# Optimization experiments

Hardware: AMD Instinct MI355X
Metric: run time of the kernel (lower is better)

The kernel has to match this reference:

```python
import jax, jax.numpy as jnp
import numpy as np

UNITS = 1024
IN_DIM = 1024
BATCH = 4096


def setup_inputs() -> dict:
    key = jax.random.key(0)
    ks = jax.random.split(key, 11)
    C = UNITS + IN_DIM  # concat dim
    glorot = lambda k, shp: jax.random.uniform(k, shp, jnp.float32, -1.0, 1.0) * np.sqrt(6.0 / (shp[0] + shp[1]))
    return {
        "inputs": jax.random.normal(ks[0], (BATCH, IN_DIM), jnp.float32),
        "hidden_state": jax.random.normal(ks[1], (BATCH, UNITS), jnp.float32),
        "cell_state": jax.random.normal(ks[2], (BATCH, UNITS), jnp.float32),
        "W_f": glorot(ks[3], (C, UNITS)), "b_f": jnp.ones((UNITS,), jnp.float32),  # forget bias init = ones
        "W_i": glorot(ks[4], (C, UNITS)), "b_i": jnp.zeros((UNITS,), jnp.float32),
        "W_c": glorot(ks[5], (C, UNITS)), "b_c": jnp.zeros((UNITS,), jnp.float32),
        "W_o": glorot(ks[6], (C, UNITS)), "b_o": jnp.zeros((UNITS,), jnp.float32),
    }


def reference(inputs, hidden_state, cell_state, W_f, b_f, W_i, b_i, W_c, b_c, W_o, b_o):
    # concat order matches original: (hidden_state, inputs)
    x = jnp.concatenate((hidden_state, inputs), axis=1)  # [B, U+D]
    f = jax.nn.sigmoid(x @ W_f + b_f)
    i = jax.nn.sigmoid(x @ W_i + b_i)
    c_cand = jnp.tanh(x @ W_c + b_c)
    new_cell = f * cell_state + i * c_cand
    o = jax.nn.sigmoid(x @ W_o + b_o)
    new_hidden = o * jnp.tanh(new_cell)
    return (new_hidden, new_cell)
```

## Files before the change

kernel.cpp:

```cpp
#include <hip/hip_runtime.h>
#include <hip/hip_bf16.h>

#define BATCH  4096
#define UNITS  1024
#define CDIM   2048
#define NDIM   4096

typedef __attribute__((ext_vector_type(8))) short bf16x8;
typedef __attribute__((ext_vector_type(4))) float f32x4;

__device__ __forceinline__ void gload_lds16(const void* g, void* l) {
    __builtin_amdgcn_global_load_lds(
        (const __attribute__((address_space(1))) unsigned int*)g,
        (__attribute__((address_space(3))) unsigned int*)l, 16, 0, 0);
}

__device__ __forceinline__ float sigm(float x) { return 1.f / (1.f + __expf(-x)); }
__device__ __forceinline__ float tanh_fast(float x) { return 2.f / (1.f + __expf(-2.f * x)) - 1.f; }

__global__ void prep(const float* __restrict__ h, const float* __restrict__ in,
                     const float* __restrict__ Wf, const float* __restrict__ Wi,
                     const float* __restrict__ Wc, const float* __restrict__ Wo,
                     __hip_bfloat16* __restrict__ x, __hip_bfloat16* __restrict__ Wt) {
    __shared__ float tile[32][33];
    int b = blockIdx.x, tid = threadIdx.x;
    if (b < (BATCH * CDIM / 4) / 256) {
        int t = b * 256 + tid;
        int col = (t % (CDIM / 4)) * 4;
        int row = t / (CDIM / 4);
        const float* src = (col < UNITS) ? (h + (size_t)row * UNITS + col)
                                         : (in + (size_t)row * UNITS + (col - UNITS));
        float4 v = *(const float4*)src;
        __hip_bfloat16* dst = x + (size_t)row * CDIM + col;
        dst[0] = __float2bfloat16(v.x); dst[1] = __float2bfloat16(v.y);
        dst[2] = __float2bfloat16(v.z); dst[3] = __float2bfloat16(v.w);
    } else {
        int idx = b - 8192;
        int g = idx >> 11, rest = idx & 2047, ky = rest >> 5, ux = rest & 31;
        const float* W = (g == 0) ? Wf : (g == 1) ? Wi : (g == 2) ? Wc : Wo;
        int u0 = ux * 32, k0 = ky * 32;
        int tx = tid & 31, ty = tid >> 5;
#pragma unroll
        for (int r = 0; r < 4; ++r)
            tile[ty + r * 8][tx] = W[(size_t)(k0 + ty + r * 8) * UNITS + u0 + tx];
        __syncthreads();
#pragma unroll
        for (int r = 0; r < 4; ++r) {
            int u = u0 + ty + r * 8;
            int n = ((u >> 5) << 7) + (((u >> 4) & 1) << 6) + (g << 4) + (u & 15);
            Wt[(size_t)n * CDIM + k0 + tx] = __float2bfloat16(tile[tx][ty + r * 8]);
        }
    }
}

__global__ __launch_bounds__(256, 2) void gemm_lstm(
    const __hip_bfloat16* __restrict__ A,
    const __hip_bfloat16* __restrict__ Bt,
    const float* __restrict__ b_f, const float* __restrict__ b_i,
    const float* __restrict__ b_c, const float* __restrict__ b_o,
    const float* __restrict__ cell,
    float* __restrict__ out)
{
    __shared__ short As[2][128 * 64];
    const int K = CDIM;

    int bid = blockIdx.x;
    int nb  = (bid & 7) * 2 + ((bid >> 3) & 1);
    int mb  = bid >> 4;
    int m0  = mb * 128, n0 = nb * 256;

    int tid  = threadIdx.x;
    int w    = tid >> 6, lane = tid & 63;
    int quad = lane >> 4, r16 = lane & 15;
    int wn   = w * 64;

    f32x4 acc[8][4];
#pragma unroll
    for (int i = 0; i < 8; ++i)
#pragma unroll
        for (int j = 0; j < 4; ++j) acc[i][j] = (f32x4){0.f, 0.f, 0.f, 0.f};

    const short* Ag = (const short*)A  + (size_t)m0 * K;
    const short* Bg = (const short*)Bt + (size_t)(n0 + wn + r16) * K + quad * 8;

    auto stageA = [&](int p, int k0) {
#pragma unroll
        for (int q = 0; q < 4; ++q) {
            int s    = q * 256 + tid;
            int row  = s >> 3;
            int cg   = (s & 7) ^ (row & 7);
            int lofs = (q * 256 + w * 64) * 8;
            gload_lds16(Ag + (size_t)row * K + k0 + cg * 8, &As[p][lofs]);
        }
    };

    bf16x8 bcur[8], bnxt[8];
#pragma unroll
    for (int ks = 0; ks < 2; ++ks)
#pragma unroll
        for (int j = 0; j < 4; ++j)
            bcur[ks * 4 + j] = *(const bf16x8*)&Bg[(size_t)(j * 16) * K + ks * 32];
    stageA(0, 0);

    for (int kt = 0; kt < K / 64; ++kt) {
        int p = kt & 1;
        asm volatile("s_waitcnt vmcnt(0)" ::: "memory");
        __syncthreads();
        if (kt + 1 < K / 64) {
            stageA(1 - p, (kt + 1) * 64);
            int kb = (kt + 1) * 64;
#pragma unroll
            for (int ks = 0; ks < 2; ++ks)
#pragma unroll
                for (int j = 0; j < 4; ++j)
                    bnxt[ks * 4 + j] = *(const bf16x8*)&Bg[(size_t)(j * 16) * K + kb + ks * 32];
        }
#pragma unroll
        for (int ks = 0; ks < 2; ++ks) {
            bf16x8 af[8];
            int kc = ((quad + ks * 4) ^ (r16 & 7)) * 8;
#pragma unroll
            for (int i = 0; i < 8; ++i)
                af[i] = *(const bf16x8*)&As[p][(i * 16 + r16) * 64 + kc];
#pragma unroll
            for (int i = 0; i < 8; ++i)
#pragma unroll
                for (int j = 0; j < 4; ++j)
                    acc[i][j] = __builtin_amdgcn_mfma_f32_16x16x32_bf16(af[i], bcur[ks * 4 + j], acc[i][j], 0, 0, 0);
        }
#pragma unroll
        for (int t = 0; t < 8; ++t) bcur[t] = bnxt[t];
    }

    int u = nb * 64 + (w >> 1) * 32 + (w & 1) * 16 + r16;
    float bfv = b_f[u], biv = b_i[u], bcv = b_c[u], bov = b_o[u];
    float* out_h = out;
    float* out_c = out + (size_t)BATCH * UNITS;
#pragma unroll
    for (int i = 0; i < 8; ++i) {
#pragma unroll
        for (int rr = 0; rr < 4; ++rr) {
            int m = m0 + i * 16 + quad * 4 + rr;
            float fg = sigm(acc[i][0][rr] + bfv);
            float ig = sigm(acc[i][1][rr] + biv);
            float cc = tanh_fast(acc[i][2][rr] + bcv);
            float og = sigm(acc[i][3][rr] + bov);
            float cold = cell[(size_t)m * UNITS + u];
            float cn = fg * cold + ig * cc;
            out_h[(size_t)m * UNITS + u] = og * tanh_fast(cn);
            out_c[(size_t)m * UNITS + u] = cn;
        }
    }
}

extern "C" void kernel_launch(void* const* d_in, const int* in_sizes, int n_in,
                              void* d_out, int out_size, void* d_ws, size_t ws_size,
                              hipStream_t stream) {
    const float* inputs = (const float*)d_in[0];
    const float* hidden = (const float*)d_in[1];
    const float* cell   = (const float*)d_in[2];
    const float* Wf = (const float*)d_in[3];
    const float* bf_ = (const float*)d_in[4];
    const float* Wi = (const float*)d_in[5];
    const float* bi_ = (const float*)d_in[6];
    const float* Wc = (const float*)d_in[7];
    const float* bc_ = (const float*)d_in[8];
    const float* Wo = (const float*)d_in[9];
    const float* bo_ = (const float*)d_in[10];
    float* out = (float*)d_out;

    char* ws = (char*)d_ws;
    __hip_bfloat16* x  = (__hip_bfloat16*)ws;
    __hip_bfloat16* Wt = (__hip_bfloat16*)(ws + (16u << 20));

    prep<<<dim3(16384), dim3(256), 0, stream>>>(hidden, inputs, Wf, Wi, Wc, Wo, x, Wt);
    gemm_lstm<<<dim3(512), dim3(256), 0, stream>>>(
        x, Wt, bf_, bi_, bc_, bo_, cell, out);
}
```

Measured before the change: 219.8 us.

## Triple-buffer A tiles with partial waitcnt and vectorize prep conversion kernel

The GEMM mainloop moves from double to triple-buffered LDS staging for A. Each step waits with a partial vmcnt instead of draining all loads, so global-to-LDS loads stay in flight across iterations, and B register loads are ping-ponged in an unrolled-by-two loop. The prep kernel now converts 8 elements per thread with 16-byte stores and transposes weights in 64x64 tiles with packed bf16x8 writes, cutting block count and store transactions. The extra LDS buffer raises shared memory per block, which may affect occupancy at 2 blocks per CU. The hand-tuned waitcnt counts must match the number of issued loads exactly.

```diff
diff --git a/kernel.cpp b/kernel.cpp
--- a/kernel.cpp
+++ b/kernel.cpp
@@ -22,33 +22,46 @@
                      const float* __restrict__ Wf, const float* __restrict__ Wi,
                      const float* __restrict__ Wc, const float* __restrict__ Wo,
                      __hip_bfloat16* __restrict__ x, __hip_bfloat16* __restrict__ Wt) {
-    __shared__ float tile[32][33];
+    __shared__ float tile[64 * 65];
     int b = blockIdx.x, tid = threadIdx.x;
-    if (b < (BATCH * CDIM / 4) / 256) {
-        int t = b * 256 + tid;
-        int col = (t % (CDIM / 4)) * 4;
-        int row = t / (CDIM / 4);
-        const float* src = (col < UNITS) ? (h + (size_t)row * UNITS + col)
-                                         : (in + (size_t)row * UNITS + (col - UNITS));
-        float4 v = *(const float4*)src;
-        __hip_bfloat16* dst = x + (size_t)row * CDIM + col;
-        dst[0] = __float2bfloat16(v.x); dst[1] = __float2bfloat16(v.y);
-        dst[2] = __float2bfloat16(v.z); dst[3] = __float2bfloat16(v.w);
+    if (b < 4096) {
+        int t   = b * 256 + tid;
+        int row = t >> 8;
+        int c8  = (t & 255) * 8;
+        const float* src = (c8 < UNITS) ? (h + (size_t)row * UNITS + c8)
+                                        : (in + (size_t)row * UNITS + (c8 - UNITS));
+        float4 v0 = *(const float4*)src;
+        float4 v1 = *(const float4*)(src + 4);
+        union { __hip_bfloat16 b[8]; bf16x8 v; } pk;
+        pk.b[0] = __float2bfloat16(v0.x); pk.b[1] = __float2bfloat16(v0.y);
+        pk.b[2] = __float2bfloat16(v0.z); pk.b[3] = __float2bfloat16(v0.w);
+        pk.b[4] = __float2bfloat16(v1.x); pk.b[5] = __float2bfloat16(v1.y);
+        pk.b[6] = __float2bfloat16(v1.z); pk.b[7] = __float2bfloat16(v1.w);
+        *(bf16x8*)(x + (size_t)row * CDIM + c8) = pk.v;
     } else {
-        int idx = b - 8192;
-        int g = idx >> 11, rest = idx & 2047, ky = rest >> 5, ux = rest & 31;
+        int idx = b - 4096;
+        int g = idx >> 9, rest = idx & 511, ky = rest >> 4, ux = rest & 15;
         const float* W = (g == 0) ? Wf : (g == 1) ? Wi : (g == 2) ? Wc : Wo;
-        int u0 = ux * 32, k0 = ky * 32;
-        int tx = tid & 31, ty = tid >> 5;
+        int k0 = ky * 64, u0 = ux * 64;
 #pragma unroll
-        for (int r = 0; r < 4; ++r)
-            tile[ty + r * 8][tx] = W[(size_t)(k0 + ty + r * 8) * UNITS + u0 + tx];
+        for (int q = 0; q < 4; ++q) {
+            int s = q * 256 + tid;
+            int row = s >> 4, c4 = s & 15;
+            float4 v = *(const float4*)&W[(size_t)(k0 + row) * UNITS + u0 + c4 * 4];
+            *(float4*)&tile[row * 65 + c4 * 4] = v;
+        }
         __syncthreads();
 #pragma unroll
-        for (int r = 0; r < 4; ++r) {
-            int u = u0 + ty + r * 8;
-            int n = ((u >> 5) << 7) + (((u >> 4) & 1) << 6) + (g << 4) + (u & 15);
-            Wt[(size_t)n * CDIM + k0 + tx] = __float2bfloat16(tile[tx][ty + r * 8]);
+        for (int q = 0; q < 2; ++q) {
+            int s = q * 256 + tid;
+            int u = s >> 3, kc = s & 7;
+            int U = u0 + u;
+            int n = ((U >> 5) << 7) + (((U >> 4) & 1) << 6) + (g << 4) + (U & 15);
+            union { __hip_bfloat16 b[8]; bf16x8 v; } pk;
+#pragma unroll
+            for (int j = 0; j < 8; ++j)
+                pk.b[j] = __float2bfloat16(tile[(kc * 8 + j) * 65 + u]);
+            *(bf16x8*)(Wt + (size_t)n * CDIM + k0 + kc * 8) = pk.v;
         }
     }
 }
@@ -61,7 +74,7 @@
     const float* __restrict__ cell,
     float* __restrict__ out)
 {
-    __shared__ short As[2][128 * 64];
+    __shared__ short As[3][128 * 64];
     const int K = CDIM;
 
     int bid = blockIdx.x;
@@ -83,53 +96,59 @@
     const short* Ag = (const short*)A  + (size_t)m0 * K;
     const short* Bg = (const short*)Bt + (size_t)(n0 + wn + r16) * K + quad * 8;
 
-    auto stageA = [&](int p, int k0) {
+    auto stageA = [&](short* dst, int k0) {
 #pragma unroll
         for (int q = 0; q < 4; ++q) {
             int s    = q * 256 + tid;
             int row  = s >> 3;
             int cg   = (s & 7) ^ (row & 7);
             int lofs = (q * 256 + w * 64) * 8;
-            gload_lds16(Ag + (size_t)row * K + k0 + cg * 8, &As[p][lofs]);
+            gload_lds16(Ag + (size_t)row * K + k0 + cg * 8, dst + lofs);
         }
     };
-
-    bf16x8 bcur[8], bnxt[8];
+    auto loadB = [&](bf16x8* dst, int k0) {
 #pragma unroll
-    for (int ks = 0; ks < 2; ++ks)
+        for (int ks = 0; ks < 2; ++ks)
 #pragma unroll
-        for (int j = 0; j < 4; ++j)
-            bcur[ks * 4 + j] = *(const bf16x8*)&Bg[(size_t)(j * 16) * K + ks * 32];
-    stageA(0, 0);
-
-    for (int kt = 0; kt < K / 64; ++kt) {
-        int p = kt & 1;
-        asm volatile("s_waitcnt vmcnt(0)" ::: "memory");
-        __syncthreads();
-        if (kt + 1 < K / 64) {
-            stageA(1 - p, (kt + 1) * 64);
-            int kb = (kt + 1) * 64;
-#pragma unroll
-            for (int ks = 0; ks < 2; ++ks)
-#pragma unroll
-                for (int j = 0; j < 4; ++j)
-                    bnxt[ks * 4 + j] = *(const bf16x8*)&Bg[(size_t)(j * 16) * K + kb + ks * 32];
-        }
+            for (int j = 0; j < 4; ++j)
+                dst[ks * 4 + j] = *(const bf16x8*)&Bg[(size_t)(j * 16) * K + k0 + ks * 32];
+    };
+    auto compute = [&](const short* pA, const bf16x8* B) {
 #pragma unroll
         for (int ks = 0; ks < 2; ++ks) {
             bf16x8 af[8];
             int kc = ((quad + ks * 4) ^ (r16 & 7)) * 8;
 #pragma unroll
             for (int i = 0; i < 8; ++i)
-                af[i] = *(const bf16x8*)&As[p][(i * 16 + r16) * 64 + kc];
+                af[i] = *(const bf16x8*)&pA[(i * 16 + r16) * 64 + kc];
 #pragma unroll
             for (int i = 0; i < 8; ++i)
 #pragma unroll
                 for (int j = 0; j < 4; ++j)
-                    acc[i][j] = __builtin_amdgcn_mfma_f32_16x16x32_bf16(af[i], bcur[ks * 4 + j], acc[i][j], 0, 0, 0);
+                    acc[i][j] = __builtin_amdgcn_mfma_f32_16x16x32_bf16(af[i], B[ks * 4 + j], acc[i][j], 0, 0, 0);
         }
-#pragma unroll
-        for (int t = 0; t < 8; ++t) bcur[t] = bnxt[t];
+    };
+
+    short *p0 = As[0], *p1 = As[1], *p2 = As[2];
+    bf16x8 B0[8], B1[8];
+    stageA(p0, 0);
+    stageA(p1, 64);
+    loadB(B0, 0);
+
+    for (int kt = 0; kt < K / 64; kt += 2) {
+        asm volatile("s_waitcnt vmcnt(12)" ::: "memory");
+        asm volatile("s_barrier" ::: "memory");
+        stageA(p2, min((kt + 2) * 64, K - 64));
+        loadB(B1, min((kt + 1) * 64, K - 64));
+        compute(p0, B0);
+        { short* t = p0; p0 = p1; p1 = p2; p2 = t; }
+
+        asm volatile("s_waitcnt vmcnt(12)" ::: "memory");
+        asm volatile("s_barrier" ::: "memory");
+        stageA(p2, min((kt + 3) * 64, K - 64));
+        loadB(B0, min((kt + 2) * 64, K - 64));
+        compute(p0, B1);
+        { short* t = p0; p0 = p1; p1 = p2; p2 = t; }
     }
 
     int u = nb * 64 + (w >> 1) * 32 + (w & 1) * 16 + r16;
@@ -173,7 +192,7 @@
     __hip_bfloat16* x  = (__hip_bfloat16*)ws;
     __hip_bfloat16* Wt = (__hip_bfloat16*)(ws + (16u << 20));
 
-    prep<<<dim3(16384), dim3(256), 0, stream>>>(hidden, inputs, Wf, Wi, Wc, Wo, x, Wt);
+    prep<<<dim3(6144), dim3(256), 0, stream>>>(hidden, inputs, Wf, Wi, Wc, Wo, x, Wt);
     gemm_lstm<<<dim3(512), dim3(256), 0, stream>>>(
         x, Wt, bf_, bi_, bc_, bo_, cell, out);
 }
```

After: 220.3 us. Within noise of the previous version (+0.2%).
